# Kernel tuning notes

Hardware: AMD Instinct MI355X
Metric: run time of the kernel (lower is better)

The kernel has to match this reference:

```python
import jax, jax.numpy as jnp
import numpy as np

WINDOW = 128  # crop size (compute_crops default window_size)


def centre_crop(centroids, window_size, h, w):
    # centroids: [C,2] int; returns flat gather coords [2, C*ws*ws]
    half = window_size // 2
    cy = jnp.clip(centroids[:, 0], half, h - half)
    cx = jnp.clip(centroids[:, 1], half, w - half)
    gy, gx = jnp.meshgrid(jnp.arange(window_size), jnp.arange(window_size), indexing='ij')
    rows = (cy - half)[:, None, None] + gy[None]  # [C,ws,ws]
    cols = (cx - half)[:, None, None] + gx[None]
    return jnp.stack([rows.reshape(-1), cols.reshape(-1)])  # [2, C*ws*ws]


def setup_inputs() -> dict:
    key = jax.random.key(0)
    ks = jax.random.split(key, 8)
    E, S, C, H, W = 6, 1, 512, 1024, 1024
    Dh = 16
    return {
        'x': jax.random.normal(ks[0], (E, H, W), dtype=jnp.float32),
        'sigma': jax.random.uniform(ks[1], (S, H, W), dtype=jnp.float32),
        'c': jax.random.normal(ks[2], (C, E), dtype=jnp.float32),
        'W1': jax.random.normal(ks[3], (E + S, Dh), dtype=jnp.float32) * 0.3,
        'b1': jnp.zeros((Dh,), dtype=jnp.float32),
        'W2': jax.random.normal(ks[4], (Dh, Dh), dtype=jnp.float32) * 0.3,
        'b2': jnp.zeros((Dh,), dtype=jnp.float32),
        'W3': jax.random.normal(ks[5], (Dh, 1), dtype=jnp.float32) * 0.3,
        'b3': jnp.zeros((1,), dtype=jnp.float32),
        'centroids_idx': jax.random.randint(ks[6], (C, 2), 0, H, dtype=jnp.int32),
    }


def reference(x, sigma, c, W1, b1, W2, b2, W3, b3, centroids_idx):
    E, h, w = x.shape
    S = sigma.shape[0]
    C = c.shape[0]
    ws = WINDOW
    mesh = centre_crop(centroids_idx, ws, h, w)  # [2, C*ws*ws]
    # gather per-instance windows from concatenated embedding+sigma maps
    xs = jnp.concatenate([x, sigma], axis=0)  # [E+S, H, W]
    g = xs[:, mesh[0], mesh[1]]               # [E+S, C*ws*ws]
    g = g.reshape(E + S, C, ws, ws).transpose(1, 0, 2, 3)  # [C, E+S, ws, ws]
    # subtract centroid descriptor from embedding channels (feature_engineering '0')
    g = jnp.concatenate([g[:, :E] - c[:, :, None, None], g[:, E:]], axis=1)
    feats = g.transpose(0, 2, 3, 1).reshape(-1, E + S)  # [(C*ws*ws), E+S]
    # per-pixel probability MLP (ProbabilityNet)
    hdn = jax.nn.relu(feats @ W1 + b1)
    hdn = jax.nn.relu(hdn @ W2 + b2)
    prob = jax.nn.sigmoid(hdn @ W3 + b3)
    prob = prob.reshape(C, 1, ws, ws)
    # instance-id / coordinate table for the downstream scatter (iidd)
    inst = jnp.repeat(jnp.arange(C, dtype=mesh.dtype), ws * ws)
    iidd = jnp.concatenate([inst[None], mesh], axis=0)  # [3, C*ws*ws]
    return prob, iidd
```

## Files before the change

### kernel.cpp

```cpp
#include <hip/hip_runtime.h>

#define WS 128
#define HW (1024 * 1024)
#define PLANE 8388608

typedef _Float16 half4 __attribute__((ext_vector_type(4)));
typedef _Float16 half8 __attribute__((ext_vector_type(8)));
typedef float floatx4 __attribute__((ext_vector_type(4)));

__global__ __launch_bounds__(256) void precompute_P(
    const float* __restrict__ x,
    const float* __restrict__ sigma,
    const float* __restrict__ W1,
    _Float16* __restrict__ P)
{
    const int px = blockIdx.x * 256 + threadIdx.x;
    float g[7];
#pragma unroll
    for (int e = 0; e < 6; ++e) g[e] = x[e * HW + px];
    g[6] = sigma[px];

    half8 lo, hi;
#pragma unroll
    for (int j = 0; j < 16; ++j) {
        float a = 0.0f;
#pragma unroll
        for (int e = 0; e < 7; ++e)
            a = fmaf(g[e], W1[e * 16 + j], a);
        if (j < 8) lo[j] = (_Float16)a; else hi[j - 8] = (_Float16)a;
    }
    *(half8*)(P + (size_t)px * 16)     = lo;
    *(half8*)(P + (size_t)px * 16 + 8) = hi;
}

__global__ __launch_bounds__(256) void instanseg_mlp(
    const _Float16* __restrict__ P,
    const float* __restrict__ c,
    const float* __restrict__ W1,
    const float* __restrict__ b1,
    const float* __restrict__ W2,
    const float* __restrict__ b2,
    const float* __restrict__ W3,
    const float* __restrict__ b3,
    const int*   __restrict__ cent,
    float* __restrict__ out)
{
    const int cid  = blockIdx.y;
    const int lane = threadIdx.x & 63;
    const int wave = threadIdx.x >> 6;
    const int quad = lane >> 4;
    const int sub  = lane & 15;

    const int cy = min(max(cent[2 * cid], 64), 960);
    const int cx = min(max(cent[2 * cid + 1], 64), 960);
    const int cy0 = cy - 64, cx0 = cx - 64;

    half4 a2;
    float w3f[4], bb2[4];
    half4 qh;
#pragma unroll
    for (int i = 0; i < 4; ++i) {
        const int k = 4 * quad + i;
        a2[i]  = (_Float16)W2[k * 16 + sub];
        w3f[i] = W3[k];
        bb2[i] = b2[k];
        float qv = -b1[k];
#pragma unroll
        for (int e = 0; e < 6; ++e)
            qv = fmaf(W1[e * 16 + k], c[cid * 6 + e], qv);
        qh[i] = (_Float16)qv;
    }
    const float b3v = b3[0];
    const floatx4 zero = {0.0f, 0.0f, 0.0f, 0.0f};

    const int wavestart = blockIdx.x * 2048 + wave * 512;

    half4 v[4], vn[4];
    {
        const int base = (cy0 + (wavestart >> 7)) * 1024 + cx0 + sub;
        const _Float16* rowp = P + (size_t)base * 16 + quad * 4;
#pragma unroll
        for (int ch = 0; ch < 4; ++ch)
            v[ch] = *(const half4*)(rowp + ch * 256);
    }

    for (int it = 0; it < 8; ++it) {
        const int start = wavestart + it * 64;

        if (it < 7) {
            const int nstart = start + 64;
            const int base = (cy0 + (nstart >> 7)) * 1024 + cx0 + (nstart & 127) + sub;
            const _Float16* rowp = P + (size_t)base * 16 + quad * 4;
#pragma unroll
            for (int ch = 0; ch < 4; ++ch)
                vn[ch] = *(const half4*)(rowp + ch * 256);
        }

        float logit[4];
#pragma unroll
        for (int ch = 0; ch < 4; ++ch) {
            half4 h = v[ch] - qh;
#pragma unroll
            for (int i = 0; i < 4; ++i)
                h[i] = h[i] > (_Float16)0.0f ? h[i] : (_Float16)0.0f;

            floatx4 c2 = __builtin_amdgcn_mfma_f32_16x16x16f16(a2, h, zero, 0, 0, 0);

            float part = 0.0f;
#pragma unroll
            for (int i = 0; i < 4; ++i)
                part = fmaf(w3f[i], fmaxf(c2[i] + bb2[i], 0.0f), part);
            part += __shfl_xor(part, 16, 64);
            part += __shfl_xor(part, 32, 64);
            logit[ch] = part;
        }

        const float l01 = (quad & 1) ? logit[1] : logit[0];
        const float l23 = (quad & 1) ? logit[3] : logit[2];
        const float lg  = (quad & 2) ? l23 : l01;
        const float prob = 1.0f / (1.0f + __expf(-(lg + b3v)));

        const int rowy = cy0 + (start >> 7);
        const int colx = cx0 + (start & 127) + lane;
        const int n    = cid * 16384 + start + lane;
        __builtin_nontemporal_store(prob,        out + n);
        __builtin_nontemporal_store((float)cid,  out + PLANE + n);
        __builtin_nontemporal_store((float)rowy, out + 2 * PLANE + n);
        __builtin_nontemporal_store((float)colx, out + 3 * PLANE + n);

        if (it < 7) {
#pragma unroll
            for (int ch = 0; ch < 4; ++ch) v[ch] = vn[ch];
        }
    }
}

extern "C" void kernel_launch(void* const* d_in, const int* in_sizes, int n_in,
                              void* d_out, int out_size, void* d_ws, size_t ws_size,
                              hipStream_t stream) {
    const float* x     = (const float*)d_in[0];
    const float* sigma = (const float*)d_in[1];
    const float* c     = (const float*)d_in[2];
    const float* W1    = (const float*)d_in[3];
    const float* b1    = (const float*)d_in[4];
    const float* W2    = (const float*)d_in[5];
    const float* b2    = (const float*)d_in[6];
    const float* W3    = (const float*)d_in[7];
    const float* b3    = (const float*)d_in[8];
    const int*   cent  = (const int*)d_in[9];
    float* out = (float*)d_out;
    _Float16* P = (_Float16*)d_ws;

    precompute_P<<<dim3(HW / 256), dim3(256), 0, stream>>>(x, sigma, W1, P);
    instanseg_mlp<<<dim3(8, 512), dim3(256), 0, stream>>>(
        P, c, W1, b1, W2, b2, W3, b3, cent, out);
}
```

Measured before the change: 214.8 us.

## Sort crops by Morton order and remap blocks for spatial L2 locality

An extra block in the precompute kernel sorts the 512 clamped centroids by Z-order (Morton) key with an O(n^2) rank sort and writes a permutation to workspace. The MLP kernel then maps blocks to crops through this permutation so that spatially close crops run together, with the block index interleaved across 8 groups. Each block now covers half a crop, 32 iterations per wave instead of 8, so the grid shrinks from 4096 to 1024 blocks. The aim is better L2/MALL reuse of the overlapping P windows. The cost is a longer serial loop per block, less parallelism, and the sort block running in the precompute launch.

```diff
diff --git a/kernel.cpp b/kernel.cpp
--- a/kernel.cpp
+++ b/kernel.cpp
@@ -3,17 +3,50 @@
 #define WS 128
 #define HW (1024 * 1024)
 #define PLANE 8388608
+#define PERM_BYTE_OFF 33554432
 
 typedef _Float16 half4 __attribute__((ext_vector_type(4)));
 typedef _Float16 half8 __attribute__((ext_vector_type(8)));
 typedef float floatx4 __attribute__((ext_vector_type(4)));
 
+__device__ inline unsigned part1by1(unsigned v) {
+    v &= 0x0000ffff;
+    v = (v ^ (v << 8)) & 0x00ff00ff;
+    v = (v ^ (v << 4)) & 0x0f0f0f0f;
+    v = (v ^ (v << 2)) & 0x33333333;
+    v = (v ^ (v << 1)) & 0x55555555;
+    return v;
+}
+
 __global__ __launch_bounds__(256) void precompute_P(
     const float* __restrict__ x,
     const float* __restrict__ sigma,
     const float* __restrict__ W1,
-    _Float16* __restrict__ P)
+    const int*   __restrict__ cent,
+    _Float16* __restrict__ P,
+    int* __restrict__ perm)
 {
+    if (blockIdx.x == 4096) {
+        __shared__ unsigned keys[512];
+        const int t = threadIdx.x;
+        for (int i = t; i < 512; i += 256) {
+            const unsigned cy = (unsigned)min(max(cent[2 * i], 64), 960);
+            const unsigned cx = (unsigned)min(max(cent[2 * i + 1], 64), 960);
+            keys[i] = (part1by1(cy) << 1) | part1by1(cx);
+        }
+        __syncthreads();
+        for (int i = t; i < 512; i += 256) {
+            const unsigned ki = keys[i];
+            int r = 0;
+            for (int j = 0; j < 512; ++j) {
+                const unsigned kj = keys[j];
+                r += (kj < ki || (kj == ki && j < i)) ? 1 : 0;
+            }
+            perm[r] = i;
+        }
+        return;
+    }
+
     const int px = blockIdx.x * 256 + threadIdx.x;
     float g[7];
 #pragma unroll
@@ -43,9 +76,16 @@
     const float* __restrict__ W3,
     const float* __restrict__ b3,
     const int*   __restrict__ cent,
+    const int*   __restrict__ perm,
     float* __restrict__ out)
 {
-    const int cid  = blockIdx.y;
+    const int lid  = blockIdx.x;
+    const int g    = lid & 7;
+    const int j    = lid >> 3;
+    const int rank = g * 64 + (j >> 1);
+    const int half = j & 1;
+    const int cid  = perm[rank];
+
     const int lane = threadIdx.x & 63;
     const int wave = threadIdx.x >> 6;
     const int quad = lane >> 4;
@@ -73,7 +113,7 @@
     const float b3v = b3[0];
     const floatx4 zero = {0.0f, 0.0f, 0.0f, 0.0f};
 
-    const int wavestart = blockIdx.x * 2048 + wave * 512;
+    const int wavestart = half * 8192 + wave * 2048;
 
     half4 v[4], vn[4];
     {
@@ -84,10 +124,10 @@
             v[ch] = *(const half4*)(rowp + ch * 256);
     }
 
-    for (int it = 0; it < 8; ++it) {
+    for (int it = 0; it < 32; ++it) {
         const int start = wavestart + it * 64;
 
-        if (it < 7) {
+        if (it < 31) {
             const int nstart = start + 64;
             const int base = (cy0 + (nstart >> 7)) * 1024 + cx0 + (nstart & 127) + sub;
             const _Float16* rowp = P + (size_t)base * 16 + quad * 4;
@@ -128,7 +168,7 @@
         __builtin_nontemporal_store((float)rowy, out + 2 * PLANE + n);
         __builtin_nontemporal_store((float)colx, out + 3 * PLANE + n);
 
-        if (it < 7) {
+        if (it < 31) {
 #pragma unroll
             for (int ch = 0; ch < 4; ++ch) v[ch] = vn[ch];
         }
@@ -150,8 +190,9 @@
     const int*   cent  = (const int*)d_in[9];
     float* out = (float*)d_out;
     _Float16* P = (_Float16*)d_ws;
+    int* perm   = (int*)((char*)d_ws + PERM_BYTE_OFF);
 
-    precompute_P<<<dim3(HW / 256), dim3(256), 0, stream>>>(x, sigma, W1, P);
-    instanseg_mlp<<<dim3(8, 512), dim3(256), 0, stream>>>(
-        P, c, W1, b1, W2, b2, W3, b3, cent, out);
+    precompute_P<<<dim3(4097), dim3(256), 0, stream>>>(x, sigma, W1, cent, P, perm);
+    instanseg_mlp<<<dim3(1024), dim3(256), 0, stream>>>(
+        P, c, W1, b1, W2, b2, W3, b3, cent, perm, out);
 }
```

New measurement: 225.4 us. 1.05x slower.
